# Kernel optimization log

Hardware: AMD Instinct MI355X
Metric: run time of the kernel (lower is better)

Reference implementation:

```python
import jax, jax.numpy as jnp
import numpy as np

TEMPERATURE = 0.07
N_BANK = 1_000_000
DIM = 128
BATCH = 1024
K_NEIGH = 200


def _prob_density(memory_bank, v, idx):
    # memory_bank: [N, D], v: [B, D] (L2-normalized), idx: [B, K]
    vals = memory_bank[idx]                      # [B, K, D] gather
    dots = jnp.einsum('bkd,bd->bk', vals, v)     # per-item dot products
    return jnp.sum(jnp.exp(dots / TEMPERATURE), axis=1)  # [B]


def setup_inputs() -> dict:
    key = jax.random.key(0)
    k1, k2, k3, k4 = jax.random.split(key, 4)
    codes = jax.random.normal(k1, (BATCH, DIM), dtype=jnp.float32)
    memory_bank = jax.random.normal(k2, (N_BANK, DIM), dtype=jnp.float32)
    # memory bank rows are unit-normalized in the LA setup
    memory_bank = memory_bank / jnp.linalg.norm(memory_bank, axis=1, keepdims=True)
    idx_background = jax.random.randint(k3, (BATCH, K_NEIGH), 0, N_BANK, dtype=jnp.int64)
    idx_close = jax.random.randint(k4, (BATCH, K_NEIGH), 0, N_BANK, dtype=jnp.int64)
    return {
        'codes': codes,
        'memory_bank': memory_bank,
        'idx_background': idx_background,
        'idx_close': idx_close,
    }


def reference(codes, memory_bank, idx_background, idx_close):
    # v = F.normalize(codes, p=2, dim=1)
    v = codes / jnp.linalg.norm(codes, axis=1, keepdims=True)
    d1 = _prob_density(memory_bank, v, idx_background)
    d2 = _prob_density(memory_bank, v, idx_close)
    # loss_cluster = log(d1) - log(d2)
    return jnp.log(d1) - jnp.log(d2)
```

## Files before the change

kernel.cpp:

```cpp
#include <hip/hip_runtime.h>
#include <math.h>


constexpr int DIM   = 128;
constexpr int KN    = 200;
constexpr int HALF  = 100;
constexpr int TROWS = 4;
constexpr int NT    = HALF / TROWS;
constexpr float INV_T = 1.0f / 0.07f;

typedef const __attribute__((address_space(1))) void gvoid_t;
typedef __attribute__((address_space(3))) void lvoid_t;

__global__ __launch_bounds__(256, 6)
void lal_kernel(const float* __restrict__ codes,
                const float* __restrict__ bank,
                const int*   __restrict__ idx_bg,
                const int*   __restrict__ idx_cl,
                float*       __restrict__ out)
{
    const int b    = blockIdx.x;
    const int tid  = threadIdx.x;
    const int w    = tid >> 6;
    const int lane = tid & 63;

    __shared__ alignas(16) float v[DIM];
    __shared__ int   s_idx[4 * HALF];
    __shared__ alignas(16) float tiles[4][3][TROWS * DIM];
    __shared__ float wsum[4];
    __shared__ float red[4];
    __shared__ float s_rnorm;

    const int* ip    = (w < 2) ? idx_bg : idx_cl;
    const int  kbase = (w & 1) * HALF;
    for (int k = lane; k < HALF; k += 64)
        s_idx[w * HALF + k] = ip[b * KN + kbase + k];

    float c  = (tid < DIM) ? codes[b * DIM + tid] : 0.0f;
    float ss = c * c;
    #pragma unroll
    for (int m = 32; m > 0; m >>= 1) ss += __shfl_xor(ss, m, 64);
    if ((tid & 63) == 0) wsum[tid >> 6] = ss;
    __syncthreads();
    if (tid == 0) {
        float t = wsum[0] + wsum[1] + wsum[2] + wsum[3];
        s_rnorm = 1.0f / sqrtf(t);
    }
    __syncthreads();
    if (tid < DIM) v[tid] = c * s_rnorm;
    __syncthreads();

    const int s = lane & 15;
    const int r = lane >> 4;
    const float4 vv0 = ((const float4*)v)[s];
    const float4 vv1 = ((const float4*)v)[s + 16];

    const float* bank_lane = bank + (lane & 31) * 4;
    const int*   midx = &s_idx[w * HALF];
    float* const tb   = &tiles[w][0][0];
    float sum = 0.0f;

    auto STAGE = [&](int t, int bsel) {
        int r0 = midx[4 * t     + (lane >> 5)];
        int r1 = midx[4 * t + 2 + (lane >> 5)];
        const float* g0 = bank_lane + (size_t)r0 * DIM;
        const float* g1 = bank_lane + (size_t)r1 * DIM;
        float* d0 = tb + bsel * (TROWS * DIM);
        float* d1 = d0 + 2 * DIM;
        __builtin_amdgcn_global_load_lds((gvoid_t*)g0, (lvoid_t*)d0, 16, 0, 0);
        __builtin_amdgcn_global_load_lds((gvoid_t*)g1, (lvoid_t*)d1, 16, 0, 0);
    };

    auto COMPUTE = [&](int bsel) {
        const float4* T = (const float4*)(tb + bsel * (TROWS * DIM));
        float4 x0 = T[r * 32 + s];
        float4 x1 = T[r * 32 + s + 16];
        float d = x0.x * vv0.x + x0.y * vv0.y + x0.z * vv0.z + x0.w * vv0.w
                + x1.x * vv1.x + x1.y * vv1.y + x1.z * vv1.z + x1.w * vv1.w;
        d += __shfl_xor(d, 1, 16);
        d += __shfl_xor(d, 2, 16);
        d += __shfl_xor(d, 4, 16);
        d += __shfl_xor(d, 8, 16);
        float e = __expf(d * INV_T);
        if (s == 0) sum += e;
    };

    STAGE(0, 0);
    STAGE(1, 1);
    int bsel = 0;
    for (int t = 0; t < NT - 2; ++t) {
        STAGE(t + 2, (bsel + 2) % 3);
        asm volatile("s_waitcnt vmcnt(4)" ::: "memory");
        COMPUTE(bsel);
        __builtin_amdgcn_sched_barrier(0);
        bsel = (bsel + 1) % 3;
    }
    asm volatile("s_waitcnt vmcnt(2)" ::: "memory");
    COMPUTE(bsel);
    bsel = (bsel + 1) % 3;
    asm volatile("s_waitcnt vmcnt(0)" ::: "memory");
    COMPUTE(bsel);

    #pragma unroll
    for (int m = 32; m > 0; m >>= 1) sum += __shfl_xor(sum, m, 64);
    if (lane == 0) red[w] = sum;
    __syncthreads();
    if (tid == 0)
        out[b] = logf(red[0] + red[1]) - logf(red[2] + red[3]);
}

extern "C" void kernel_launch(void* const* d_in, const int* in_sizes, int n_in,
                              void* d_out, int out_size, void* d_ws, size_t ws_size,
                              hipStream_t stream)
{
    const float* codes  = (const float*)d_in[0];
    const float* bank   = (const float*)d_in[1];
    const int*   idx_bg = (const int*)d_in[2];
    const int*   idx_cl = (const int*)d_in[3];
    float*       out    = (float*)d_out;

    const int batch = in_sizes[0] / DIM;
    lal_kernel<<<batch, 256, 0, stream>>>(codes, bank, idx_bg, idx_cl, out);
}
```

Baseline: 590.6 us.

## Invert gather into a full bank stream with per-row reference linked lists

Replaces the per-batch random row gather with a multi-kernel pipeline. It builds a head/next linked list from each bank row to the (batch, neighbour) entries that reference it, streams the entire memory bank sequentially, and chases each row's list. Each hit computes the dot product and atomically accumulates exp(d/T) into per-batch sums, and a final kernel applies the logs. This swaps ~400K scattered 512-byte gathers for a coalesced read of the whole 512MB bank, at the cost of extra launches, a head-array init, atomics and divergent list chasing. The new path only runs when the workspace is at least 16MB; otherwise the old kernel is used.

```diff
diff --git a/kernel.cpp b/kernel.cpp
--- a/kernel.cpp
+++ b/kernel.cpp
@@ -2,22 +2,136 @@
 #include <math.h>
 
 
-constexpr int DIM   = 128;
-constexpr int KN    = 200;
+constexpr int   DIM   = 128;
+constexpr int   KN    = 200;
+constexpr int   NBANK = 1000000;
+constexpr float INV_T = 1.0f / 0.07f;
+
+
+__global__ __launch_bounds__(256)
+void k_init(int* __restrict__ head, float* __restrict__ dacc, int batch)
+{
+    const int i = blockIdx.x * blockDim.x + threadIdx.x;
+    const int n = gridDim.x * blockDim.x;
+    for (int r = i; r < NBANK; r += n) head[r] = -1;
+    if (i < 2 * batch) dacc[i] = 0.0f;
+}
+
+__global__ __launch_bounds__(128)
+void k_vnorm(const float* __restrict__ codes, float* __restrict__ vtab)
+{
+    const int b = blockIdx.x;
+    const int t = threadIdx.x;
+    __shared__ float w[2];
+    float c  = codes[b * DIM + t];
+    float ss = c * c;
+    #pragma unroll
+    for (int m = 32; m > 0; m >>= 1) ss += __shfl_xor(ss, m, 64);
+    if ((t & 63) == 0) w[t >> 6] = ss;
+    __syncthreads();
+    const float rn = 1.0f / sqrtf(w[0] + w[1]);
+    vtab[b * DIM + t] = c * rn;
+}
+
+__global__ __launch_bounds__(256)
+void k_build(const int* __restrict__ idx_bg, const int* __restrict__ idx_cl,
+             int* __restrict__ head, int* __restrict__ next, int batch)
+{
+    const int n  = 2 * batch * KN;
+    const int bk = batch * KN;
+    for (int e = blockIdx.x * blockDim.x + threadIdx.x; e < n;
+         e += gridDim.x * blockDim.x) {
+        const int r = (e < bk) ? idx_bg[e] : idx_cl[e - bk];
+        next[e] = atomicExch(&head[r], e);
+    }
+}
+
+__global__ __launch_bounds__(256)
+void k_main(const float* __restrict__ bank, const int* __restrict__ head,
+            const int* __restrict__ next, const float* __restrict__ vtab,
+            float* __restrict__ dacc, int batch)
+{
+    const int seg  = blockIdx.x;
+    const int tid  = threadIdx.x;
+    const int base = seg * 512;
+    const int bk   = batch * KN;
+
+    __shared__ int s_head[512];
+    for (int i = tid; i < 512; i += 256) {
+        const int r = base + i;
+        s_head[i] = (r < NBANK) ? head[r] : -1;
+    }
+    __syncthreads();
+
+    const int w    = tid >> 6;
+    const int lane = tid & 63;
+    const int half = lane >> 5;
+    const int sl   = lane & 31;
+
+    auto ldrow = [&](int j) -> float4 {
+        const int r = base + 8 * j + 2 * w + half;
+        return (r < NBANK) ? ((const float4*)(bank + (size_t)r * DIM))[sl]
+                           : make_float4(0.f, 0.f, 0.f, 0.f);
+    };
+
+    auto chase = [&](int j, float4 x) {
+        const int lr = 8 * j + 2 * w + half;
+        int e = s_head[lr];
+        while (__any(e >= 0)) {
+            const bool act = (e >= 0);
+            int   en = -1, di = 0;
+            float4 vb = make_float4(0.f, 0.f, 0.f, 0.f);
+            if (act) {
+                const int list = (e >= bk) ? 1 : 0;
+                const int b    = (e - list * bk) / KN;
+                di = list * batch + b;
+                vb = ((const float4*)(vtab + (size_t)b * DIM))[sl];
+                en = next[e];
+            }
+            float d = x.x * vb.x + x.y * vb.y + x.z * vb.z + x.w * vb.w;
+            d += __shfl_xor(d, 16, 32);
+            d += __shfl_xor(d, 8, 32);
+            d += __shfl_xor(d, 4, 32);
+            d += __shfl_xor(d, 2, 32);
+            d += __shfl_xor(d, 1, 32);
+            if (act && sl == 0) atomicAdd(&dacc[di], __expf(d * INV_T));
+            e = en;
+        }
+    };
+
+    for (int j = 0; j < 64; j += 4) {
+        float4 xa = ldrow(j);
+        float4 xb = ldrow(j + 1);
+        float4 xc = ldrow(j + 2);
+        float4 xd = ldrow(j + 3);
+        chase(j,     xa);
+        chase(j + 1, xb);
+        chase(j + 2, xc);
+        chase(j + 3, xd);
+    }
+}
+
+__global__ __launch_bounds__(256)
+void k_fin(const float* __restrict__ dacc, float* __restrict__ out, int batch)
+{
+    const int b = blockIdx.x * blockDim.x + threadIdx.x;
+    if (b < batch) out[b] = logf(dacc[b]) - logf(dacc[batch + b]);
+}
+
+
 constexpr int HALF  = 100;
 constexpr int TROWS = 4;
 constexpr int NT    = HALF / TROWS;
-constexpr float INV_T = 1.0f / 0.07f;
 
 typedef const __attribute__((address_space(1))) void gvoid_t;
 typedef __attribute__((address_space(3))) void lvoid_t;
 
 __global__ __launch_bounds__(256, 6)
-void lal_kernel(const float* __restrict__ codes,
-                const float* __restrict__ bank,
-                const int*   __restrict__ idx_bg,
-                const int*   __restrict__ idx_cl,
-                float*       __restrict__ out)
+void lal_fallback(const float* __restrict__ codes,
+                  const float* __restrict__ bank,
+                  const int*   __restrict__ idx_bg,
+                  const int*   __restrict__ idx_cl,
+                  float*       __restrict__ out)
 {
     const int b    = blockIdx.x;
     const int tid  = threadIdx.x;
@@ -70,7 +184,6 @@
         __builtin_amdgcn_global_load_lds((gvoid_t*)g0, (lvoid_t*)d0, 16, 0, 0);
         __builtin_amdgcn_global_load_lds((gvoid_t*)g1, (lvoid_t*)d1, 16, 0, 0);
     };
-
     auto COMPUTE = [&](int bsel) {
         const float4* T = (const float4*)(tb + bsel * (TROWS * DIM));
         float4 x0 = T[r * 32 + s];
@@ -109,6 +222,7 @@
         out[b] = logf(red[0] + red[1]) - logf(red[2] + red[3]);
 }
 
+
 extern "C" void kernel_launch(void* const* d_in, const int* in_sizes, int n_in,
                               void* d_out, int out_size, void* d_ws, size_t ws_size,
                               hipStream_t stream)
@@ -120,5 +234,21 @@
     float*       out    = (float*)d_out;
 
     const int batch = in_sizes[0] / DIM;
-    lal_kernel<<<batch, 256, 0, stream>>>(codes, bank, idx_bg, idx_cl, out);
-}
+
+    if (ws_size >= (size_t)(16u << 20)) {
+        char*  ws   = (char*)d_ws;
+        int*   head = (int*)(ws);
+        int*   next = (int*)(ws + (4u << 20));
+        float* vtab = (float*)(ws + (8u << 20));
+        float* dacc = (float*)(ws + (12u << 20));
+
+        k_init <<<2048, 256, 0, stream>>>(head, dacc, batch);
+        k_vnorm<<<batch, 128, 0, stream>>>(codes, vtab);
+        k_build<<<(2 * batch * KN + 255) / 256, 256, 0, stream>>>(
+            idx_bg, idx_cl, head, next, batch);
+        k_main <<<2048, 256, 0, stream>>>(bank, head, next, vtab, dacc, batch);
+        k_fin  <<<(batch + 255) / 256, 256, 0, stream>>>(dacc, out, batch);
+    } else {
+        lal_fallback<<<batch, 256, 0, stream>>>(codes, bank, idx_bg, idx_cl, out);
+    }
+}
```

Result: slower. 694.3 us (+17.6%).
